# Kernel optimization log

Hardware: AMD Instinct MI355X
Metric: run time of the kernel (lower is better)

## Reference

```python
import jax, jax.numpy as jnp
import numpy as np

HIDDEN = 512
TEMPERATURE = float(np.sqrt(HIDDEN))  # scaled-dot temperature
BATCH = 64


def _build_weights(attn_weight, N, K):
    """Vectorized version of get_attn_weight: (S,S,H) with S = N*K+1.
    Regions: 0=same_sample, 1=same_class, 2=diff_class, 3=support->query,
    4=query->support, 5=query->query. Replicates the torch overwrite order."""
    S = N * K + 1
    NK = N * K
    i = jnp.arange(S)[:, None]
    j = jnp.arange(S)[None, :]
    idx = jnp.full((S, S), 2, dtype=jnp.int32)                      # w_diff_class
    idx = jnp.where((i // K) == (j // K), 1, idx)                   # w_same_class
    idx = jnp.where((i < NK) & (j == NK), 3, idx)                   # w_stoquery
    idx = jnp.where(i == j, 0, idx)                                 # w_same_sample (diag)
    idx = jnp.where((i == NK) & (j < NK), 4, idx)                   # w_querytos
    idx = jnp.where((i == NK) & (j == NK), 5, idx)                  # w_query
    return attn_weight[idx]  # (S, S, H)


def setup_inputs() -> dict:
    key = jax.random.key(0)
    kq, kk, kv, kw = jax.random.split(key, 4)
    N, K = 10, 10
    S = N * K + 1  # 101
    q = jax.random.normal(kq, (BATCH, S, HIDDEN), dtype=jnp.float32)
    k = jax.random.normal(kk, (BATCH, S, HIDDEN), dtype=jnp.float32)
    v = jax.random.normal(kv, (BATCH, S, HIDDEN), dtype=jnp.float32)
    bound = float(np.sqrt(6 / 2))
    attn_weight = jax.random.uniform(kw, (6, HIDDEN), dtype=jnp.float32,
                                     minval=-bound, maxval=bound)
    return {"q": q, "k": k, "v": v, "attn_weight": attn_weight, "N": N, "K": K}


def reference(q, k, v, attn_weight, N, K):
    # attn[b,i,j] = softmax_j(q.k^T / temperature)
    scores = jnp.einsum("bih,bjh->bij", q, k) / TEMPERATURE
    attn = jax.nn.softmax(scores, axis=2)  # dropout p=0 (eval) -> identity
    weights = _build_weights(attn_weight, N, K)  # (S,S,H)
    # out[b,i,h] = sum_j attn[b,i,j] * weights[i,j,h] * v[b,j,h]
    out = jnp.einsum("bij,ijh,bjh->bih", attn, weights, v)
    return out, attn
```

## Files before the change

### kernel.cpp

```cpp
#include <hip/hip_runtime.h>
#include <math.h>
#include <stdint.h>

#define BATCH 64
#define SEQ   101
#define HID   512
#define NKQ   100
#define KCLS  10
#define INV_TEMP 0.04419417382415922f

typedef short bf16x8 __attribute__((ext_vector_type(8)));
typedef float f32x4  __attribute__((ext_vector_type(4)));

__device__ inline void split_bf16(float x, short& hi, short& lo) {
    uint32_t u = __builtin_bit_cast(uint32_t, x);
    hi = (short)(u >> 16);
    float hf = __builtin_bit_cast(float, u & 0xFFFF0000u);
    float l  = x - hf;
    lo = (short)(__builtin_bit_cast(uint32_t, l) >> 16);
}

__global__ __launch_bounds__(512, 4)
void qk_softmax(const float* __restrict__ q, const float* __restrict__ k,
                float* __restrict__ attn, float* __restrict__ apad) {
    __shared__ float sc[16][132];
    const int b   = blockIdx.x & 63;
    const int i0  = (blockIdx.x >> 6) * 16;
    const int tid = threadIdx.x;
    const int wv  = tid >> 6, lane = tid & 63;
    const int m   = lane & 15;
    const int kq  = (lane >> 4) * 8;
    const int rq  = (lane >> 4) * 4;

    const float* qb = q + (size_t)b * SEQ * HID;
    const float* kb = k + (size_t)b * SEQ * HID;

    {
        const int j0w = wv * 16;
        int qrow = i0 + m;  if (qrow > NKQ) qrow = NKQ;
        int krow = j0w + m; if (krow > NKQ) krow = NKQ;
        const float* qr = qb + (size_t)qrow * HID + kq;
        const float* kr = kb + (size_t)krow * HID + kq;
        f32x4 acc = {};
        #pragma unroll 4
        for (int ks = 0; ks < HID; ks += 32) {
            float4 a0 = *(const float4*)(qr + ks);
            float4 a1 = *(const float4*)(qr + ks + 4);
            float4 b0 = *(const float4*)(kr + ks);
            float4 b1 = *(const float4*)(kr + ks + 4);
            float xa[8] = {a0.x,a0.y,a0.z,a0.w,a1.x,a1.y,a1.z,a1.w};
            float xb[8] = {b0.x,b0.y,b0.z,b0.w,b1.x,b1.y,b1.z,b1.w};
            bf16x8 aH, aL, bH, bL;
            #pragma unroll
            for (int e = 0; e < 8; ++e) { short h,l; split_bf16(xa[e],h,l); aH[e]=h; aL[e]=l; }
            #pragma unroll
            for (int e = 0; e < 8; ++e) { short h,l; split_bf16(xb[e],h,l); bH[e]=h; bL[e]=l; }
            acc = __builtin_amdgcn_mfma_f32_16x16x32_bf16(aH, bH, acc, 0, 0, 0);
            acc = __builtin_amdgcn_mfma_f32_16x16x32_bf16(aH, bL, acc, 0, 0, 0);
            acc = __builtin_amdgcn_mfma_f32_16x16x32_bf16(aL, bH, acc, 0, 0, 0);
        }
        #pragma unroll
        for (int r = 0; r < 4; ++r)
            sc[rq + r][j0w + m] = acc[r];
    }
    __syncthreads();

    {
        const int row = tid >> 5, t32 = tid & 31;
        const int gi  = i0 + row;
        float mx = -1e30f;
        for (int j = t32; j < SEQ; j += 32) {
            float s = sc[row][j] * INV_TEMP;
            sc[row][j] = s;
            mx = fmaxf(mx, s);
        }
        #pragma unroll
        for (int off = 1; off < 32; off <<= 1) mx = fmaxf(mx, __shfl_xor(mx, off));
        float sum = 0.f;
        for (int j = t32; j < SEQ; j += 32) {
            float e = __expf(sc[row][j] - mx);
            sc[row][j] = e;
            sum += e;
        }
        #pragma unroll
        for (int off = 1; off < 32; off <<= 1) sum += __shfl_xor(sum, off);
        const float inv = 1.f / sum;
        if (gi < SEQ) {
            float* arow = attn + ((size_t)b * SEQ + gi) * SEQ;
            float* prow = apad + ((size_t)b * SEQ + gi) * 128;
            for (int j = t32; j < SEQ; j += 32) {
                float a = sc[row][j] * inv;
                arow[j] = a;
                prow[j] = a;
            }
            for (int j = SEQ + t32; j < 128; j += 32) prow[j] = 0.f;
        }
    }
}

#define VR 36
#define VT 144

__global__ __launch_bounds__(512, 6)
void pv_out(const float* __restrict__ v, const float* __restrict__ aw,
            const float* __restrict__ apad, float* __restrict__ out) {
    __shared__ float vraw[SEQ][VR];
    __shared__ short vth[32][VT];
    __shared__ short vtl[32][VT];
    const int b   = blockIdx.x & 63;
    const int h0  = (blockIdx.x >> 6) * 32;
    const int tid = threadIdx.x;
    const int wv  = tid >> 6, lane = tid & 63;
    const int m   = lane & 15;
    const int kq  = (lane >> 4) * 8;
    const int rq  = (lane >> 4) * 4;

    const float* vb = v + (size_t)b * SEQ * HID + h0;
    for (int f = tid; f < SEQ * 8; f += 512) {
        int r = f >> 3, c = (f & 7) << 2;
        *(float4*)&vraw[r][c] = *(const float4*)(vb + (size_t)r * HID + c);
    }
    __syncthreads();
    for (int it2 = tid; it2 < 32 * 36; it2 += 512) {
        int h = it2 & 31, j = (it2 >> 5) << 2;
        short4 hv, lv;
        split_bf16(j + 0 < SEQ ? vraw[j + 0][h] : 0.f, hv.x, lv.x);
        split_bf16(j + 1 < SEQ ? vraw[j + 1][h] : 0.f, hv.y, lv.y);
        split_bf16(j + 2 < SEQ ? vraw[j + 2][h] : 0.f, hv.z, lv.z);
        split_bf16(j + 3 < SEQ ? vraw[j + 3][h] : 0.f, hv.w, lv.w);
        *(short4*)&vth[h][j] = hv;
        *(short4*)&vtl[h][j] = lv;
    }
    __syncthreads();

    if (wv < 7) {
        const int i0 = wv * 16;
        int ai = i0 + m; if (ai > NKQ) ai = NKQ;
        const int ci = ai / KCLS;
        const float* ar = apad + ((size_t)b * SEQ + ai) * 128 + kq;
        f32x4 T[2] = {}, U[2] = {};
        #pragma unroll
        for (int ks = 0; ks < 4; ++ks) {
            float4 u0 = *(const float4*)(ar + ks * 32);
            float4 u1 = *(const float4*)(ar + ks * 32 + 4);
            float x[8] = {u0.x,u0.y,u0.z,u0.w,u1.x,u1.y,u1.z,u1.w};
            bf16x8 Ah, Al, Mh;
            #pragma unroll
            for (int e = 0; e < 8; ++e) {
                short h, l; split_bf16(x[e], h, l);
                Ah[e] = h; Al[e] = l;
                const int j = ks * 32 + kq + e;
                Mh[e] = ((j / KCLS) == ci) ? h : (short)0;
            }
            #pragma unroll
            for (int ht = 0; ht < 2; ++ht) {
                const bf16x8 Bh = *(const bf16x8*)&vth[ht * 16 + m][ks * 32 + kq];
                const bf16x8 Bl = *(const bf16x8*)&vtl[ht * 16 + m][ks * 32 + kq];
                T[ht] = __builtin_amdgcn_mfma_f32_16x16x32_bf16(Ah, Bh, T[ht], 0, 0, 0);
                T[ht] = __builtin_amdgcn_mfma_f32_16x16x32_bf16(Ah, Bl, T[ht], 0, 0, 0);
                T[ht] = __builtin_amdgcn_mfma_f32_16x16x32_bf16(Al, Bh, T[ht], 0, 0, 0);
                U[ht] = __builtin_amdgcn_mfma_f32_16x16x32_bf16(Mh, Bh, U[ht], 0, 0, 0);
            }
        }
        const float* ap = apad + (size_t)b * SEQ * 128;
        #pragma unroll
        for (int ht = 0; ht < 2; ++ht) {
            const int hl = ht * 16 + m;
            const int h  = h0 + hl;
            const float w0 = aw[0 * HID + h], w1 = aw[1 * HID + h], w2 = aw[2 * HID + h];
            const float w3 = aw[3 * HID + h], w4 = aw[4 * HID + h], w5 = aw[5 * HID + h];
            const float vN = vraw[NKQ][hl];
            #pragma unroll
            for (int r = 0; r < 4; ++r) {
                const int i = i0 + rq + r;
                if (i >= SEQ) continue;
                const float t = T[ht][r], u = U[ht][r];
                const float aiN = ap[(size_t)i * 128 + NKQ];
                float o;
                if (i < NKQ) {
                    const float aii = ap[(size_t)i * 128 + i];
                    const float vi  = vraw[i][hl];
                    o = w2 * t + (w1 - w2) * u + (w0 - w1) * aii * vi + (w3 - w2) * aiN * vN;
                } else {
                    o = w4 * t + (w5 - w4) * aiN * vN;
                }
                out[((size_t)b * SEQ + i) * HID + h] = o;
            }
        }
    }
}

extern "C" void kernel_launch(void* const* d_in, const int* in_sizes, int n_in,
                              void* d_out, int out_size, void* d_ws, size_t ws_size,
                              hipStream_t stream) {
    const float* q  = (const float*)d_in[0];
    const float* k  = (const float*)d_in[1];
    const float* v  = (const float*)d_in[2];
    const float* aw = (const float*)d_in[3];
    float* out  = (float*)d_out;
    float* attn = out + (size_t)BATCH * SEQ * HID;
    float* apad = (float*)d_ws;

    qk_softmax<<<dim3(448), dim3(512), 0, stream>>>(q, k, attn, apad);
    pv_out<<<dim3(1024), dim3(512), 0, stream>>>(v, aw, apad, out);
}
```

Before: 126.5 us.

## Stage Q/K chunks in LDS and drop K low-part MFMA using RTN bf16

The QK^T kernel now loads 64-wide chunks of K (as round-to-nearest bf16) and Q (as hi/lo bf16 split) into shared memory, so all waves share the staged data instead of each fetching and splitting rows from global memory. The K low-part correction MFMA is removed, leaving two MFMAs per step instead of three. This targets redundant global loads, redundant conversion work and MFMA count. In exchange it adds two barriers per chunk and lowers the precision of the scores, which could affect tolerance.

```diff
diff --git a/kernel.cpp b/kernel.cpp
--- a/kernel.cpp
+++ b/kernel.cpp
@@ -19,10 +19,20 @@
     float l  = x - hf;
     lo = (short)(__builtin_bit_cast(uint32_t, l) >> 16);
 }
+__device__ inline short rtn_bf16(float x) {
+    uint32_t u = __builtin_bit_cast(uint32_t, x);
+    return (short)((u + 0x7FFFu + ((u >> 16) & 1u)) >> 16);
+}
+
+#define KCH 64
+#define KST 72
 
 __global__ __launch_bounds__(512, 4)
 void qk_softmax(const float* __restrict__ q, const float* __restrict__ k,
                 float* __restrict__ attn, float* __restrict__ apad) {
+    __shared__ short khi[128][KST];
+    __shared__ short qhi[16][KST];
+    __shared__ short qlo[16][KST];
     __shared__ float sc[16][132];
     const int b   = blockIdx.x & 63;
     const int i0  = (blockIdx.x >> 6) * 16;
@@ -31,38 +41,51 @@
     const int m   = lane & 15;
     const int kq  = (lane >> 4) * 8;
     const int rq  = (lane >> 4) * 4;
+    const int j0w = wv * 16;
 
     const float* qb = q + (size_t)b * SEQ * HID;
     const float* kb = k + (size_t)b * SEQ * HID;
 
-    {
-        const int j0w = wv * 16;
-        int qrow = i0 + m;  if (qrow > NKQ) qrow = NKQ;
-        int krow = j0w + m; if (krow > NKQ) krow = NKQ;
-        const float* qr = qb + (size_t)qrow * HID + kq;
-        const float* kr = kb + (size_t)krow * HID + kq;
-        f32x4 acc = {};
-        #pragma unroll 4
-        for (int ks = 0; ks < HID; ks += 32) {
-            float4 a0 = *(const float4*)(qr + ks);
-            float4 a1 = *(const float4*)(qr + ks + 4);
-            float4 b0 = *(const float4*)(kr + ks);
-            float4 b1 = *(const float4*)(kr + ks + 4);
-            float xa[8] = {a0.x,a0.y,a0.z,a0.w,a1.x,a1.y,a1.z,a1.w};
-            float xb[8] = {b0.x,b0.y,b0.z,b0.w,b1.x,b1.y,b1.z,b1.w};
-            bf16x8 aH, aL, bH, bL;
-            #pragma unroll
-            for (int e = 0; e < 8; ++e) { short h,l; split_bf16(xa[e],h,l); aH[e]=h; aL[e]=l; }
-            #pragma unroll
-            for (int e = 0; e < 8; ++e) { short h,l; split_bf16(xb[e],h,l); bH[e]=h; bL[e]=l; }
-            acc = __builtin_amdgcn_mfma_f32_16x16x32_bf16(aH, bH, acc, 0, 0, 0);
-            acc = __builtin_amdgcn_mfma_f32_16x16x32_bf16(aH, bL, acc, 0, 0, 0);
-            acc = __builtin_amdgcn_mfma_f32_16x16x32_bf16(aL, bH, acc, 0, 0, 0);
-        }
-        #pragma unroll
-        for (int r = 0; r < 4; ++r)
-            sc[rq + r][j0w + m] = acc[r];
-    }
+    f32x4 acc = {};
+    for (int kc = 0; kc < HID; kc += KCH) {
+        #pragma unroll
+        for (int s = 0; s < 4; ++s) {
+            const int f = tid + s * 512;
+            const int r = f >> 4, c = (f & 15) << 2;
+            float4 x = make_float4(0.f, 0.f, 0.f, 0.f);
+            if (r < SEQ) x = *(const float4*)(kb + (size_t)r * HID + kc + c);
+            short4 hv;
+            hv.x = rtn_bf16(x.x); hv.y = rtn_bf16(x.y);
+            hv.z = rtn_bf16(x.z); hv.w = rtn_bf16(x.w);
+            *(short4*)&khi[r][c] = hv;
+        }
+        if (tid < 256) {
+            const int r = tid >> 4, c = (tid & 15) << 2;
+            const int gi = i0 + r;
+            float4 x = make_float4(0.f, 0.f, 0.f, 0.f);
+            if (gi < SEQ) x = *(const float4*)(qb + (size_t)gi * HID + kc + c);
+            short4 hv, lv;
+            split_bf16(x.x, hv.x, lv.x);
+            split_bf16(x.y, hv.y, lv.y);
+            split_bf16(x.z, hv.z, lv.z);
+            split_bf16(x.w, hv.w, lv.w);
+            *(short4*)&qhi[r][c] = hv;
+            *(short4*)&qlo[r][c] = lv;
+        }
+        __syncthreads();
+        #pragma unroll
+        for (int ks = 0; ks < KCH; ks += 32) {
+            const bf16x8 qH = *(const bf16x8*)&qhi[m][ks + kq];
+            const bf16x8 qL = *(const bf16x8*)&qlo[m][ks + kq];
+            const bf16x8 kH = *(const bf16x8*)&khi[j0w + m][ks + kq];
+            acc = __builtin_amdgcn_mfma_f32_16x16x32_bf16(qH, kH, acc, 0, 0, 0);
+            acc = __builtin_amdgcn_mfma_f32_16x16x32_bf16(qL, kH, acc, 0, 0, 0);
+        }
+        __syncthreads();
+    }
+    #pragma unroll
+    for (int r = 0; r < 4; ++r)
+        sc[rq + r][j0w + m] = acc[r];
     __syncthreads();
 
     {
```

Result: faster. 119.4 us (-5.6%).
